# Kernel optimization log

Hardware: AMD Instinct MI355X
Metric: run time of the kernel (lower is better)

Reference implementation:

```python
import jax, jax.numpy as jnp
import numpy as np

N, E, D = 100000, 1600000, 64
BN_EPS = 1e-5
ATT_SLOPE = 0.2   # GATConv attention leaky relu slope
ACT_SLOPE = 0.01  # nn.LeakyReLU default


def setup_inputs() -> dict:
    key = jax.random.key(0)
    ks = jax.random.split(key, 12)
    s = 1.0 / np.sqrt(D)
    return {
        "x": jax.random.normal(ks[0], (N, D), jnp.float32),
        "W1": jax.random.normal(ks[1], (D, D), jnp.float32) * s,
        "att_src1": jax.random.normal(ks[2], (D,), jnp.float32) * s,
        "att_dst1": jax.random.normal(ks[3], (D,), jnp.float32) * s,
        "bias1": jnp.zeros((D,), jnp.float32),
        "bn_gamma": jnp.ones((D,), jnp.float32),
        "bn_beta": jnp.zeros((D,), jnp.float32),
        "W2": jax.random.normal(ks[4], (D, D), jnp.float32) * s,
        "att_src2": jax.random.normal(ks[5], (D,), jnp.float32) * s,
        "att_dst2": jax.random.normal(ks[6], (D,), jnp.float32) * s,
        "bias2": jnp.zeros((D,), jnp.float32),
        "edge_index": jax.random.randint(ks[7], (2, E), 0, N, jnp.int64 if jax.config.jax_enable_x64 else jnp.int32),
    }


def gat_conv(x, src, dst, W, a_src, a_dst, bias):
    # h: [N, D] transformed features
    h = x @ W
    # per-edge attention logits (gather of per-node scores)
    logit = jax.nn.leaky_relu((h @ a_src)[src] + (h @ a_dst)[dst], ATT_SLOPE)
    # segment softmax over incoming edges of each destination node
    m = jax.ops.segment_max(logit, dst, num_segments=N)
    e = jnp.exp(logit - m[dst])
    z = jax.ops.segment_sum(e, dst, num_segments=N)
    alpha = e / z[dst]                              # [E']
    msg = h[src] * alpha[:, None]                   # [E', D] gather + weight
    return jax.ops.segment_sum(msg, dst, num_segments=N) + bias


def reference(x, W1, att_src1, att_dst1, bias1, bn_gamma, bn_beta,
              W2, att_src2, att_dst2, bias2, edge_index):
    # PyG GATConv adds self-loops by default
    loops = jnp.arange(N, dtype=edge_index.dtype)
    src = jnp.concatenate([edge_index[0], loops])
    dst = jnp.concatenate([edge_index[1], loops])

    x0 = x
    h = gat_conv(x, src, dst, W1, att_src1, att_dst1, bias1)
    # BatchNorm1d in training mode: batch stats, biased variance
    mu = h.mean(axis=0)
    var = h.var(axis=0)
    h = (h - mu) * jax.lax.rsqrt(var + BN_EPS) * bn_gamma + bn_beta
    h = jax.nn.leaky_relu(h, ACT_SLOPE)
    # dropout p=0.0 -> no-op
    out = gat_conv(h, src, dst, W2, att_src2, att_dst2, bias2)
    # mean over stacked [input x, final node_emb]
    return 0.5 * (x0 + out)
```

## Files before the change

### kernel.cpp

```cpp
#include <hip/hip_runtime.h>
#include <math.h>

#define D 64
#define CAP 64
#define NBB 128
#define NPB 64
#define NBINMAX 2048

__device__ __forceinline__ float lrelu(float x, float s) { return x > 0.f ? x : s * x; }

__device__ __forceinline__ unsigned f2bf(float f) {
    unsigned b = __builtin_bit_cast(unsigned, f);
    return (b + 0x7fffu + ((b >> 16) & 1u)) >> 16;
}
__device__ __forceinline__ float bflo(unsigned u) { return __builtin_bit_cast(float, u << 16); }
__device__ __forceinline__ float bfhi(unsigned u) { return __builtin_bit_cast(float, u & 0xffff0000u); }

__device__ __forceinline__ void mm_rows(const float* __restrict__ xin,
        const float* __restrict__ W, const float* __restrict__ a_src, const float* __restrict__ a_dst,
        const float* __restrict__ bn_sum, const float* __restrict__ bn_sumsq,
        const float* __restrict__ gamma, const float* __restrict__ beta, int apply_bn,
        unsigned* __restrict__ hb, float* __restrict__ ssrc, float* __restrict__ sdst,
        int N, int worker, int nworkers, int lane, int wv) {
    float w[D];
    #pragma unroll
    for (int k = 0; k < D; ++k) w[k] = W[k * D + lane];
    float asv = a_src[lane], adv = a_dst[lane];
    float sc = 1.f, sh = 0.f;
    if (apply_bn) {
        float mu = bn_sum[lane] / (float)N;
        float var = bn_sumsq[lane] / (float)N - mu * mu;
        float rs = rsqrtf(var + 1e-5f);
        sc = rs * gamma[lane];
        sh = beta[lane] - mu * sc;
    }
    for (int r = worker * 4 + wv; r < N; r += nworkers * 4) {
        float v = xin[(size_t)r * D + lane];
        if (apply_bn) { v = v * sc + sh; v = v > 0.f ? v : 0.01f * v; }
        int vi = __builtin_bit_cast(int, v);
        float a0 = 0.f, a1 = 0.f, a2 = 0.f, a3 = 0.f;
        #pragma unroll
        for (int k = 0; k < D; k += 4) {
            float b0 = __builtin_bit_cast(float, __builtin_amdgcn_readlane(vi, k + 0));
            float b1 = __builtin_bit_cast(float, __builtin_amdgcn_readlane(vi, k + 1));
            float b2 = __builtin_bit_cast(float, __builtin_amdgcn_readlane(vi, k + 2));
            float b3 = __builtin_bit_cast(float, __builtin_amdgcn_readlane(vi, k + 3));
            a0 = fmaf(b0, w[k + 0], a0);
            a1 = fmaf(b1, w[k + 1], a1);
            a2 = fmaf(b2, w[k + 2], a2);
            a3 = fmaf(b3, w[k + 3], a3);
        }
        float acc = (a0 + a1) + (a2 + a3);
        float accp = __shfl_xor(acc, 1, 64);
        unsigned packed = f2bf(acc) | (f2bf(accp) << 16);
        if (!(lane & 1)) hb[(size_t)r * 32 + (lane >> 1)] = packed;
        float v1 = acc * asv, v2 = acc * adv;
        #pragma unroll
        for (int off = 32; off; off >>= 1) {
            v1 += __shfl_xor(v1, off, 64);
            v2 += __shfl_xor(v2, off, 64);
        }
        if (lane == 0) { ssrc[r] = v1; sdst[r] = v2; }
    }
}

__global__ __launch_bounds__(256) void k_bin_mm1(const int* __restrict__ ei, int E,
        int* __restrict__ bin_ptr, unsigned* __restrict__ binned, int BCAP,
        const float* __restrict__ xin, const float* __restrict__ W,
        const float* __restrict__ a_src, const float* __restrict__ a_dst,
        unsigned* __restrict__ hb, float* __restrict__ ssrc, float* __restrict__ sdst, int N) {
    __shared__ int hist[NBINMAX], cur[NBINMAX];
    int tid = threadIdx.x, lane = tid & 63, wv = tid >> 6;
    if (blockIdx.x < NBB) {
        int nb = (N + NPB - 1) >> 6;
        for (int t = tid; t < nb; t += 256) hist[t] = 0;
        __syncthreads();
        int nq4 = E >> 2;
        int qpb = (nq4 + NBB - 1) / NBB;
        int q0 = blockIdx.x * qpb;
        int q1 = q0 + qpb; if (q1 > nq4) q1 = nq4;
        const int4* s4 = (const int4*)ei;
        const int4* d4 = (const int4*)(ei + E);
        for (int i = q0 + tid; i < q1; i += 256) {
            int4 d = d4[i];
            atomicAdd(&hist[d.x >> 6], 1);
            atomicAdd(&hist[d.y >> 6], 1);
            atomicAdd(&hist[d.z >> 6], 1);
            atomicAdd(&hist[d.w >> 6], 1);
        }
        if (blockIdx.x == 0 && tid < (E & 3)) {
            int dd = ei[E + (nq4 << 2) + tid];
            atomicAdd(&hist[dd >> 6], 1);
        }
        __syncthreads();
        for (int t = tid; t < nb; t += 256)
            cur[t] = hist[t] ? atomicAdd(&bin_ptr[t], hist[t]) : 0;
        __syncthreads();
        for (int i = q0 + tid; i < q1; i += 256) {
            int4 s = s4[i];
            int4 d = d4[i];
            int t0 = d.x >> 6, t1 = d.y >> 6, t2 = d.z >> 6, t3 = d.w >> 6;
            int p0 = atomicAdd(&cur[t0], 1);
            int p1 = atomicAdd(&cur[t1], 1);
            int p2 = atomicAdd(&cur[t2], 1);
            int p3 = atomicAdd(&cur[t3], 1);
            if (p0 < BCAP) binned[(size_t)t0 * BCAP + p0] = (unsigned)s.x | ((unsigned)(d.x & 63) << 17);
            if (p1 < BCAP) binned[(size_t)t1 * BCAP + p1] = (unsigned)s.y | ((unsigned)(d.y & 63) << 17);
            if (p2 < BCAP) binned[(size_t)t2 * BCAP + p2] = (unsigned)s.z | ((unsigned)(d.z & 63) << 17);
            if (p3 < BCAP) binned[(size_t)t3 * BCAP + p3] = (unsigned)s.w | ((unsigned)(d.w & 63) << 17);
        }
        if (blockIdx.x == 0 && tid < (E & 3)) {
            int i = (nq4 << 2) + tid;
            int ss = ei[i], dd = ei[E + i];
            int t = dd >> 6;
            int p = atomicAdd(&cur[t], 1);
            if (p < BCAP) binned[(size_t)t * BCAP + p] = (unsigned)ss | ((unsigned)(dd & 63) << 17);
        }
    } else {
        mm_rows(xin, W, a_src, a_dst, nullptr, nullptr, nullptr, nullptr, 0,
                hb, ssrc, sdst, N, blockIdx.x - NBB, gridDim.x - NBB, lane, wv);
    }
}

__global__ __launch_bounds__(256) void k_mm_att(const float* __restrict__ xin,
        const float* __restrict__ W, const float* __restrict__ a_src, const float* __restrict__ a_dst,
        const float* __restrict__ bn_sum, const float* __restrict__ bn_sumsq,
        const float* __restrict__ gamma, const float* __restrict__ beta,
        unsigned* __restrict__ hb, float* __restrict__ ssrc, float* __restrict__ sdst, int N) {
    int tid = threadIdx.x, lane = tid & 63, wv = tid >> 6;
    mm_rows(xin, W, a_src, a_dst, bn_sum, bn_sumsq, gamma, beta, 1,
            hb, ssrc, sdst, N, blockIdx.x, gridDim.x, lane, wv);
}

#define AGG_ISSUE(P, q) { \
    int sA_ = __shfl(sal0.x, (q), 16), sB_ = __shfl(sal0.y, (q), 16); \
    int sC_ = __shfl(sal0.z, (q), 16), sD_ = __shfl(sal0.w, (q), 16); \
    P##A = h2[(size_t)sA_ * 16 + sl]; P##B = h2[(size_t)sB_ * 16 + sl]; \
    P##C = h2[(size_t)sC_ * 16 + sl]; P##D = h2[(size_t)sD_ * 16 + sl]; }

#define AGG_CONSUME(P, i) { \
    float eA_ = __shfl(e0, (i), 16), eB_ = __shfl(e1, (i), 16); \
    float eC_ = __shfl(e2, (i), 16), eD_ = __shfl(e3, (i), 16); \
    acc.x = fmaf(eA_, bflo(P##A.x), acc.x); acc.y = fmaf(eA_, bfhi(P##A.x), acc.y); \
    acc.z = fmaf(eA_, bflo(P##A.y), acc.z); acc.w = fmaf(eA_, bfhi(P##A.y), acc.w); \
    acc.x = fmaf(eB_, bflo(P##B.x), acc.x); acc.y = fmaf(eB_, bfhi(P##B.x), acc.y); \
    acc.z = fmaf(eB_, bflo(P##B.y), acc.z); acc.w = fmaf(eB_, bfhi(P##B.y), acc.w); \
    acc.x = fmaf(eC_, bflo(P##C.x), acc.x); acc.y = fmaf(eC_, bfhi(P##C.x), acc.y); \
    acc.z = fmaf(eC_, bflo(P##C.y), acc.z); acc.w = fmaf(eC_, bfhi(P##C.y), acc.w); \
    acc.x = fmaf(eD_, bflo(P##D.x), acc.x); acc.y = fmaf(eD_, bfhi(P##D.x), acc.y); \
    acc.z = fmaf(eD_, bflo(P##D.y), acc.z); acc.w = fmaf(eD_, bfhi(P##D.y), acc.w); }

__global__ __launch_bounds__(256) void k_agg(const unsigned* __restrict__ binned,
        const int* __restrict__ bin_ptr, int BCAP,
        const float* __restrict__ ssrc, const float* __restrict__ sdst,
        const unsigned* __restrict__ hb, const float* __restrict__ bias,
        const float* __restrict__ x, float* __restrict__ out,
        float* __restrict__ bn_sum, float* __restrict__ bn_sumsq, int mode, int N) {
    __shared__ int colL[NPB][CAP];
    __shared__ int cntL[NPB];
    __shared__ float ssL[NPB], sdL[NPB];
    __shared__ float sbn1[D], sbn2[D];
    int tid = threadIdx.x;
    int sl = tid & 15;
    int g = tid >> 4;
    int b = blockIdx.x;
    int n0 = b << 6;

    if (tid < NPB) {
        cntL[tid] = 0;
        int nd = n0 + tid;
        ssL[tid] = (nd < N) ? ssrc[nd] : 0.f;
        sdL[tid] = (nd < N) ? sdst[nd] : 0.f;
    }
    if (mode == 0 && tid < D) { sbn1[tid] = 0.f; sbn2[tid] = 0.f; }
    __syncthreads();

    int m = bin_ptr[b]; if (m > BCAP) m = BCAP;
    {
        const unsigned* base = binned + (size_t)b * BCAP;
        for (int i = tid; i < m; i += 256) {
            unsigned e = base[i];
            int dl = (int)(e >> 17);
            int k = atomicAdd(&cntL[dl], 1);
            if (k < CAP) colL[dl][k] = (int)(e & 0x1FFFFu);
        }
    }
    __syncthreads();

    const uint2* h2 = (const uint2*)hb;
    float4 s1 = make_float4(0, 0, 0, 0), s2 = make_float4(0, 0, 0, 0);

    auto loadSal = [&](int d, int& dg, int4& sal) {
        int dgl = cntL[d]; if (dgl > CAP) dgl = CAP;
        int4 c = ((const int4*)colL[d])[sl];
        int eb = sl << 2;
        int nd = n0 + d;
        int self = (nd < N) ? nd : 0;
        sal.x = (eb + 0 < dgl) ? c.x : self;
        sal.y = (eb + 1 < dgl) ? c.y : self;
        sal.z = (eb + 2 < dgl) ? c.z : self;
        sal.w = (eb + 3 < dgl) ? c.w : self;
        dg = dgl;
    };

    int dg0; int4 sal0;
    loadSal(g, dg0, sal0);
    float4 g0;
    g0.x = ssrc[sal0.x]; g0.y = ssrc[sal0.y];
    g0.z = ssrc[sal0.z]; g0.w = ssrc[sal0.w];

    #pragma unroll
    for (int idx = 0; idx < 4; ++idx) {
        int d = g + (idx << 4);
        int nd = n0 + d;
        int ndc = (nd < N) ? nd : 0;
        uint2 hv = h2[(size_t)ndc * 16 + sl];
        int Q = dg0 > 0 ? ((dg0 + 3) >> 2) : 1;
        uint2 p0A, p0B, p0C, p0D, p1A, p1B, p1C, p1D, p2A, p2B, p2C, p2D;
        AGG_ISSUE(p0, 0)
        if (Q > 1) AGG_ISSUE(p1, 1)
        if (Q > 2) AGG_ISSUE(p2, 2)

        int dg1 = 0; int4 sal1 = make_int4(0, 0, 0, 0);
        float4 g1 = make_float4(0, 0, 0, 0);
        if (idx < 3) {
            loadSal(d + 16, dg1, sal1);
            g1.x = ssrc[sal1.x]; g1.y = ssrc[sal1.y];
            g1.z = ssrc[sal1.z]; g1.w = ssrc[sal1.w];
        }

        float sdn = sdL[d];
        int eb = sl << 2;
        float e0 = (eb + 0 < dg0) ? __expf(lrelu(g0.x + sdn, 0.2f)) : 0.f;
        float e1 = (eb + 1 < dg0) ? __expf(lrelu(g0.y + sdn, 0.2f)) : 0.f;
        float e2 = (eb + 2 < dg0) ? __expf(lrelu(g0.z + sdn, 0.2f)) : 0.f;
        float e3 = (eb + 3 < dg0) ? __expf(lrelu(g0.w + sdn, 0.2f)) : 0.f;
        float z = (e0 + e1) + (e2 + e3);
        #pragma unroll
        for (int off = 1; off <= 8; off <<= 1) z += __shfl_xor(z, off, 64);
        float es = __expf(lrelu(ssL[d] + sdn, 0.2f));
        z += es;
        float4 acc;
        acc.x = es * bflo(hv.x); acc.y = es * bfhi(hv.x);
        acc.z = es * bflo(hv.y); acc.w = es * bfhi(hv.y);

        int i = 0;
        while (true) {
            AGG_CONSUME(p0, i)
            if (i + 3 < Q) AGG_ISSUE(p0, i + 3)
            if (++i >= Q) break;
            AGG_CONSUME(p1, i)
            if (i + 3 < Q) AGG_ISSUE(p1, i + 3)
            if (++i >= Q) break;
            AGG_CONSUME(p2, i)
            if (i + 3 < Q) AGG_ISSUE(p2, i + 3)
            if (++i >= Q) break;
        }

        if (nd < N) {
            float inv = 1.f / z;
            float4 b4 = ((const float4*)bias)[sl];
            float4 v;
            v.x = acc.x * inv + b4.x; v.y = acc.y * inv + b4.y;
            v.z = acc.z * inv + b4.z; v.w = acc.w * inv + b4.w;
            if (mode == 0) {
                ((float4*)out)[(size_t)nd * 16 + sl] = v;
                s1.x += v.x; s1.y += v.y; s1.z += v.z; s1.w += v.w;
                s2.x += v.x * v.x; s2.y += v.y * v.y;
                s2.z += v.z * v.z; s2.w += v.w * v.w;
            } else {
                float4 xv = ((const float4*)x)[(size_t)nd * 16 + sl];
                v.x = 0.5f * (xv.x + v.x); v.y = 0.5f * (xv.y + v.y);
                v.z = 0.5f * (xv.z + v.z); v.w = 0.5f * (xv.w + v.w);
                ((float4*)out)[(size_t)nd * 16 + sl] = v;
            }
        }
        dg0 = dg1; sal0 = sal1; g0 = g1;
    }
    if (mode == 0) {
        int c = sl * 4;
        atomicAdd(&sbn1[c + 0], s1.x); atomicAdd(&sbn1[c + 1], s1.y);
        atomicAdd(&sbn1[c + 2], s1.z); atomicAdd(&sbn1[c + 3], s1.w);
        atomicAdd(&sbn2[c + 0], s2.x); atomicAdd(&sbn2[c + 1], s2.y);
        atomicAdd(&sbn2[c + 2], s2.z); atomicAdd(&sbn2[c + 3], s2.w);
        __syncthreads();
        if (tid < D) {
            atomicAdd(&bn_sum[tid], sbn1[tid]);
            atomicAdd(&bn_sumsq[tid], sbn2[tid]);
        }
    }
}

extern "C" void kernel_launch(void* const* d_in, const int* in_sizes, int n_in,
                              void* d_out, int out_size, void* d_ws, size_t ws_size,
                              hipStream_t stream) {
    const float* x     = (const float*)d_in[0];
    const float* W1    = (const float*)d_in[1];
    const float* as1   = (const float*)d_in[2];
    const float* ad1   = (const float*)d_in[3];
    const float* b1    = (const float*)d_in[4];
    const float* gamma = (const float*)d_in[5];
    const float* beta  = (const float*)d_in[6];
    const float* W2    = (const float*)d_in[7];
    const float* as2   = (const float*)d_in[8];
    const float* ad2   = (const float*)d_in[9];
    const float* b2    = (const float*)d_in[10];
    const int*   ei    = (const int*)d_in[11];
    int N = in_sizes[0] / D;
    int E = in_sizes[11] / 2;
    float* out = (float*)d_out;

    float* ws = (float*)d_ws;
    unsigned* hb = (unsigned*)ws;
    float* ssrc = (float*)(hb + (size_t)N * 32);
    float* sdst = ssrc + N;
    int* binp   = (int*)(sdst + N);
    float* bn   = (float*)(binp + NBINMAX);
    unsigned* binned = (unsigned*)(bn + 128);

    int nb = (N + NPB - 1) >> 6;
    int BCAP = E / nb + (E / nb) / 4 + 256;

    dim3 blk(256);

    hipMemsetAsync(binp, 0, NBINMAX * 4 + 512, stream);

    k_bin_mm1<<<2048, blk, 0, stream>>>(ei, E, binp, binned, BCAP,
                                        x, W1, as1, ad1, hb, ssrc, sdst, N);

    k_agg<<<nb, blk, 0, stream>>>(binned, binp, BCAP, ssrc, sdst, hb, b1,
                                  nullptr, out, bn, bn + 64, 0, N);

    k_mm_att<<<2048, blk, 0, stream>>>(out, W2, as2, ad2, bn, bn + 64, gamma, beta,
                                       hb, ssrc, sdst, N);
    k_agg<<<nb, blk, 0, stream>>>(binned, binp, BCAP, ssrc, sdst, hb, b2,
                                  x, out, bn, bn + 64, 1, N);
}
```

Measured before the change: 286.1 us.

## Compute node feature transform with bf16 MFMA tiles instead of scalar readlane FMAs

```diff
diff --git a/kernel.cpp b/kernel.cpp
--- a/kernel.cpp
+++ b/kernel.cpp
@@ -7,6 +7,9 @@
 #define NPB 64
 #define NBINMAX 2048
 
+typedef __attribute__((ext_vector_type(8))) short bf16x8;
+typedef __attribute__((ext_vector_type(4))) float f32x4;
+
 __device__ __forceinline__ float lrelu(float x, float s) { return x > 0.f ? x : s * x; }
 
 __device__ __forceinline__ unsigned f2bf(float f) {
@@ -16,51 +19,102 @@
 __device__ __forceinline__ float bflo(unsigned u) { return __builtin_bit_cast(float, u << 16); }
 __device__ __forceinline__ float bfhi(unsigned u) { return __builtin_bit_cast(float, u & 0xffff0000u); }
 
-__device__ __forceinline__ void mm_rows(const float* __restrict__ xin,
+__device__ __forceinline__ void mm_mfma(const float* __restrict__ xin,
         const float* __restrict__ W, const float* __restrict__ a_src, const float* __restrict__ a_dst,
         const float* __restrict__ bn_sum, const float* __restrict__ bn_sumsq,
         const float* __restrict__ gamma, const float* __restrict__ beta, int apply_bn,
         unsigned* __restrict__ hb, float* __restrict__ ssrc, float* __restrict__ sdst,
-        int N, int worker, int nworkers, int lane, int wv) {
-    float w[D];
+        int N, int wave, int nwaves, int lane) {
+    int row16 = lane & 15;
+    int kg = lane >> 4;
+
+    bf16x8 wf[2][4];
     #pragma unroll
-    for (int k = 0; k < D; ++k) w[k] = W[k * D + lane];
-    float asv = a_src[lane], adv = a_dst[lane];
-    float sc = 1.f, sh = 0.f;
+    for (int kc = 0; kc < 2; ++kc)
+        #pragma unroll
+        for (int jb = 0; jb < 4; ++jb) {
+            bf16x8 f;
+            #pragma unroll
+            for (int e = 0; e < 8; ++e)
+                f[e] = (short)f2bf(W[(kc * 32 + kg * 8 + e) * D + jb * 16 + row16]);
+            wf[kc][jb] = f;
+        }
+    float asv[4], adv[4];
+    #pragma unroll
+    for (int jb = 0; jb < 4; ++jb) {
+        asv[jb] = a_src[jb * 16 + row16];
+        adv[jb] = a_dst[jb * 16 + row16];
+    }
+    float sc[2][8], sh[2][8];
     if (apply_bn) {
-        float mu = bn_sum[lane] / (float)N;
-        float var = bn_sumsq[lane] / (float)N - mu * mu;
-        float rs = rsqrtf(var + 1e-5f);
-        sc = rs * gamma[lane];
-        sh = beta[lane] - mu * sc;
-    }
-    for (int r = worker * 4 + wv; r < N; r += nworkers * 4) {
-        float v = xin[(size_t)r * D + lane];
-        if (apply_bn) { v = v * sc + sh; v = v > 0.f ? v : 0.01f * v; }
-        int vi = __builtin_bit_cast(int, v);
-        float a0 = 0.f, a1 = 0.f, a2 = 0.f, a3 = 0.f;
-        #pragma unroll
-        for (int k = 0; k < D; k += 4) {
-            float b0 = __builtin_bit_cast(float, __builtin_amdgcn_readlane(vi, k + 0));
-            float b1 = __builtin_bit_cast(float, __builtin_amdgcn_readlane(vi, k + 1));
-            float b2 = __builtin_bit_cast(float, __builtin_amdgcn_readlane(vi, k + 2));
-            float b3 = __builtin_bit_cast(float, __builtin_amdgcn_readlane(vi, k + 3));
-            a0 = fmaf(b0, w[k + 0], a0);
-            a1 = fmaf(b1, w[k + 1], a1);
-            a2 = fmaf(b2, w[k + 2], a2);
-            a3 = fmaf(b3, w[k + 3], a3);
-        }
-        float acc = (a0 + a1) + (a2 + a3);
-        float accp = __shfl_xor(acc, 1, 64);
-        unsigned packed = f2bf(acc) | (f2bf(accp) << 16);
-        if (!(lane & 1)) hb[(size_t)r * 32 + (lane >> 1)] = packed;
-        float v1 = acc * asv, v2 = acc * adv;
-        #pragma unroll
-        for (int off = 32; off; off >>= 1) {
-            v1 += __shfl_xor(v1, off, 64);
-            v2 += __shfl_xor(v2, off, 64);
-        }
-        if (lane == 0) { ssrc[r] = v1; sdst[r] = v2; }
+        #pragma unroll
+        for (int kc = 0; kc < 2; ++kc)
+            #pragma unroll
+            for (int e = 0; e < 8; ++e) {
+                int c = kc * 32 + kg * 8 + e;
+                float mu = bn_sum[c] / (float)N;
+                float var = bn_sumsq[c] / (float)N - mu * mu;
+                float rs = rsqrtf(var + 1e-5f);
+                sc[kc][e] = rs * gamma[c];
+                sh[kc][e] = beta[c] - mu * sc[kc][e];
+            }
+    }
+
+    int ntiles = (N + 15) >> 4;
+    for (int t = wave; t < ntiles; t += nwaves) {
+        int r0 = t << 4;
+        int arow = r0 + row16;
+        int arowc = arow < N ? arow : N - 1;
+        bf16x8 af[2];
+        #pragma unroll
+        for (int kc = 0; kc < 2; ++kc) {
+            const float* p = xin + (size_t)arowc * D + kc * 32 + kg * 8;
+            float4 u0 = *(const float4*)p;
+            float4 u1 = *(const float4*)(p + 4);
+            float v[8] = {u0.x, u0.y, u0.z, u0.w, u1.x, u1.y, u1.z, u1.w};
+            bf16x8 f;
+            #pragma unroll
+            for (int e = 0; e < 8; ++e) {
+                float vv = v[e];
+                if (apply_bn) { vv = vv * sc[kc][e] + sh[kc][e]; vv = vv > 0.f ? vv : 0.01f * vv; }
+                f[e] = (short)f2bf(vv);
+            }
+            af[kc] = f;
+        }
+        f32x4 acc0 = {0,0,0,0}, acc1 = {0,0,0,0}, acc2 = {0,0,0,0}, acc3 = {0,0,0,0};
+        acc0 = __builtin_amdgcn_mfma_f32_16x16x32_bf16(af[0], wf[0][0], acc0, 0, 0, 0);
+        acc1 = __builtin_amdgcn_mfma_f32_16x16x32_bf16(af[0], wf[0][1], acc1, 0, 0, 0);
+        acc2 = __builtin_amdgcn_mfma_f32_16x16x32_bf16(af[0], wf[0][2], acc2, 0, 0, 0);
+        acc3 = __builtin_amdgcn_mfma_f32_16x16x32_bf16(af[0], wf[0][3], acc3, 0, 0, 0);
+        acc0 = __builtin_amdgcn_mfma_f32_16x16x32_bf16(af[1], wf[1][0], acc0, 0, 0, 0);
+        acc1 = __builtin_amdgcn_mfma_f32_16x16x32_bf16(af[1], wf[1][1], acc1, 0, 0, 0);
+        acc2 = __builtin_amdgcn_mfma_f32_16x16x32_bf16(af[1], wf[1][2], acc2, 0, 0, 0);
+        acc3 = __builtin_amdgcn_mfma_f32_16x16x32_bf16(af[1], wf[1][3], acc3, 0, 0, 0);
+
+        #pragma unroll
+        for (int r = 0; r < 4; ++r) {
+            int row = r0 + kg * 4 + r;
+            float c0 = acc0[r], c1 = acc1[r], c2 = acc2[r], c3 = acc3[r];
+            float p0 = __shfl_xor(c0, 1, 64);
+            float p1 = __shfl_xor(c1, 1, 64);
+            float p2 = __shfl_xor(c2, 1, 64);
+            float p3 = __shfl_xor(c3, 1, 64);
+            if (!(row16 & 1) && row < N) {
+                size_t hbase = (size_t)row * 32 + (row16 >> 1);
+                hb[hbase + 0]  = f2bf(c0) | (f2bf(p0) << 16);
+                hb[hbase + 8]  = f2bf(c1) | (f2bf(p1) << 16);
+                hb[hbase + 16] = f2bf(c2) | (f2bf(p2) << 16);
+                hb[hbase + 24] = f2bf(c3) | (f2bf(p3) << 16);
+            }
+            float vs = fmaf(c0, asv[0], fmaf(c1, asv[1], fmaf(c2, asv[2], c3 * asv[3])));
+            float vd = fmaf(c0, adv[0], fmaf(c1, adv[1], fmaf(c2, adv[2], c3 * adv[3])));
+            #pragma unroll
+            for (int off = 1; off <= 8; off <<= 1) {
+                vs += __shfl_xor(vs, off, 64);
+                vd += __shfl_xor(vd, off, 64);
+            }
+            if (row16 == 0 && row < N) { ssrc[row] = vs; sdst[row] = vd; }
+        }
     }
 }
 
@@ -117,8 +171,10 @@
             if (p < BCAP) binned[(size_t)t * BCAP + p] = (unsigned)ss | ((unsigned)(dd & 63) << 17);
         }
     } else {
-        mm_rows(xin, W, a_src, a_dst, nullptr, nullptr, nullptr, nullptr, 0,
-                hb, ssrc, sdst, N, blockIdx.x - NBB, gridDim.x - NBB, lane, wv);
+        int wave = (blockIdx.x - NBB) * 4 + wv;
+        int nwaves = (gridDim.x - NBB) * 4;
+        mm_mfma(xin, W, a_src, a_dst, nullptr, nullptr, nullptr, nullptr, 0,
+                hb, ssrc, sdst, N, wave, nwaves, lane);
     }
 }
 
@@ -128,8 +184,8 @@
         const float* __restrict__ gamma, const float* __restrict__ beta,
         unsigned* __restrict__ hb, float* __restrict__ ssrc, float* __restrict__ sdst, int N) {
     int tid = threadIdx.x, lane = tid & 63, wv = tid >> 6;
-    mm_rows(xin, W, a_src, a_dst, bn_sum, bn_sumsq, gamma, beta, 1,
-            hb, ssrc, sdst, N, blockIdx.x, gridDim.x, lane, wv);
+    mm_mfma(xin, W, a_src, a_dst, bn_sum, bn_sumsq, gamma, beta, 1,
+            hb, ssrc, sdst, N, blockIdx.x * 4 + wv, gridDim.x * 4, lane);
 }
 
 #define AGG_ISSUE(P, q) { \
@@ -331,7 +387,7 @@
     k_agg<<<nb, blk, 0, stream>>>(binned, binp, BCAP, ssrc, sdst, hb, b1,
                                   nullptr, out, bn, bn + 64, 0, N);
 
-    k_mm_att<<<2048, blk, 0, stream>>>(out, W2, as2, ad2, bn, bn + 64, gamma, beta,
+    k_mm_att<<<1024, blk, 0, stream>>>(out, W2, as2, ad2, bn, bn + 64, gamma, beta,
                                        hb, ssrc, sdst, N);
     k_agg<<<nb, blk, 0, stream>>>(binned, binp, BCAP, ssrc, sdst, hb, b2,
                                   x, out, bn, bn + 64, 1, N);
```

Result: faster. 246.1 us (-14.0%).
